# Optimization experiments

Measured on AMD Instinct MI355X. Metric: run time of the kernel, lower is better.

Reference implementation:

```python
import jax, jax.numpy as jnp
import numpy as np

TIME_SEG_LEN = 5
PRED_STEPS = 1
B, N, D = 4, 4096, 4
F1, F2 = 32, 64  # cnn filters; F2 must equal GCSConv/Dense width 64


def _conv1d_time(x, Wc1, bc1, Wc2, bc2):
    # x: [B, N, T, D] -> per-node temporal CNN collapsing T=5 -> 1 -> [B, N, F2]
    b, n, t, d = x.shape
    xr = x.reshape(b * n, t, d)
    dn = ('NWC', 'WIO', 'NWC')
    h = jax.lax.conv_general_dilated(xr, Wc1, (1,), 'VALID', dimension_numbers=dn) + bc1
    h = jax.nn.relu(h)
    h = jax.lax.conv_general_dilated(h, Wc2, (1,), 'VALID', dimension_numbers=dn) + bc2
    return h.reshape(b, n, -1)  # [B, N, F2]


def setup_inputs() -> dict:
    key = jax.random.key(0)
    ks = jax.random.split(key, 12)
    time_segs = jax.random.normal(ks[0], (B, TIME_SEG_LEN, N, D), dtype=jnp.float32)
    edges = jax.random.randint(ks[1], (N, N), 0, 2, dtype=jnp.int32)
    s = lambda *sh: 1.0 / np.sqrt(sh[-2] if len(sh) > 1 else sh[0])
    return {
        'time_segs': time_segs,
        'edges': edges,
        'Wc1': jax.random.normal(ks[2], (3, D, F1), dtype=jnp.float32) * 0.3,
        'bc1': jnp.zeros((F1,), jnp.float32),
        'Wc2': jax.random.normal(ks[3], (3, F1, F2), dtype=jnp.float32) * 0.1,
        'bc2': jnp.zeros((F2,), jnp.float32),
        'Wg1': jax.random.normal(ks[4], (F2, 64), dtype=jnp.float32) * 0.125,
        'bg': jnp.zeros((64,), jnp.float32),
        'Wd': jax.random.normal(ks[5], (F2 + 64, 64), dtype=jnp.float32) * 0.09,
        'bd': jnp.zeros((64,), jnp.float32),
        'Wo': jax.random.normal(ks[6], (64, D), dtype=jnp.float32) * 0.125,
        'bo': jnp.zeros((D,), jnp.float32),
    }


def reference(time_segs, edges, Wc1, bc1, Wc2, bc2, Wg1, bg, Wd, bd, Wo, bo):
    A = edges.astype(jnp.float32)
    n = A.shape[0]
    deg = jnp.sum(A, axis=-1, keepdims=True)              # row degree
    A_norm = A / jnp.where(deg > 0, deg, 1.0)             # D^-1 A (symmetric=False)
    A_nd = A_norm * (1.0 - jnp.eye(n, dtype=A.dtype))     # self-edge masking of X row j == zeroing diag
    col_deg = jnp.sum(A, axis=0)                          # e = np.sum(edges, axis=0)
    alive = (col_deg != 0).astype(time_segs.dtype)[None, :, None]  # zero-degree nodes -> zeros branch

    ext = jnp.transpose(time_segs, (0, 2, 1, 3))          # [B, N, T, D]
    for i in range(PRED_STEPS):
        seg = ext[:, :, i:, :]                            # [B, N, 5, D]
        cond = _conv1d_time(seg, Wc1, bc1, Wc2, bc2)      # [B, N, F2]
        # Vectorized per-node masked GCSConv: row j of tanh(A X_j W1 + X_j W2 + b)
        # with X_j = X zeroed at node j. Skip term vanishes at row j.
        agg = jnp.einsum('jk,bkf->bjf', A_nd, cond)       # [B, N, F2]
        G = jnp.tanh(agg @ Wg1 + bg) * alive              # [B, N, 64]
        h = jax.nn.relu(jnp.concatenate([cond, G], axis=-1) @ Wd + bd)
        nxt = seg[:, :, -1, :] + jnp.tanh(h @ Wo + bo)    # residual update [B, N, D]
        ext = jnp.concatenate([ext, nxt[:, :, None, :]], axis=2)
    out = jnp.transpose(ext, (0, 2, 1, 3))                # [B, T+P, N, D]
    return out[:, TIME_SEG_LEN:, :, :]                    # [B, pred_steps, N, D]
```

## Files before the change

kernel.cpp:

```cpp
#include <hip/hip_runtime.h>

typedef unsigned short ushort_t;
typedef unsigned int uint_t;
typedef unsigned long long u64_t;
typedef __attribute__((ext_vector_type(8))) __bf16 bf16x8;
typedef __attribute__((ext_vector_type(4))) float f32x4;

#define NN 4096
#define TT 5
#define F1 32
#define F2 64

__device__ __forceinline__ ushort_t f2bf(float x) {
    union { float f; uint_t u; } v; v.f = x;
    uint_t r = (v.u + 0x7FFFu + ((v.u >> 16) & 1u)) >> 16;
    return (ushort_t)r;
}
__device__ __forceinline__ float bf16f(float x) {
    union { float f; uint_t u; } v; v.f = x;
    v.u = (v.u + 0x7FFFu + ((v.u >> 16) & 1u)) & 0xFFFF0000u;
    return v.f;
}

__global__ __launch_bounds__(256) void k1_cond(
    const float* __restrict__ ts, const float* __restrict__ Wc1, const float* __restrict__ bc1,
    const float* __restrict__ Wc2, const float* __restrict__ bc2,
    float* __restrict__ condf, ushort_t* __restrict__ condT)
{
    const int b = blockIdx.y;
    const int j0 = blockIdx.x * 32;
    const int t = threadIdx.x;

    __shared__ float sWc1[384];
    __shared__ float sbc1[F1];
    __shared__ float sWc2[96 * F2];
    __shared__ float sbc2[F2];
    __shared__ float sh1[4][96];
    __shared__ ushort_t scb[64][40];

    for (int i = t; i < 384; i += 256) sWc1[i] = Wc1[i];
    for (int i = t; i < 96 * F2; i += 256) sWc2[i] = Wc2[i];
    if (t < F1) sbc1[t] = bc1[t];
    if (t < F2) sbc2[t] = bc2[t];
    __syncthreads();

    const int sub = t >> 6, lane = t & 63;
    for (int c = 0; c < 8; ++c) {
        const int n = c * 4 + sub;
        const int j = j0 + n;
        for (int idx = lane; idx < 96; idx += 64) {
            const int tt0 = idx >> 5, f1 = idx & 31;
            float a = sbc1[f1];
            #pragma unroll
            for (int dt = 0; dt < 3; ++dt) {
                const float4 x = *(const float4*)(ts + (((b * TT + tt0 + dt) * NN) + j) * 4);
                a += x.x * sWc1[(dt * 4 + 0) * F1 + f1];
                a += x.y * sWc1[(dt * 4 + 1) * F1 + f1];
                a += x.z * sWc1[(dt * 4 + 2) * F1 + f1];
                a += x.w * sWc1[(dt * 4 + 3) * F1 + f1];
            }
            sh1[sub][idx] = fmaxf(a, 0.f);
        }
        __syncthreads();
        {
            float cacc = sbc2[lane];
            #pragma unroll 8
            for (int e = 0; e < 96; ++e) cacc += sh1[sub][e] * sWc2[e * F2 + lane];
            condf[(((b << 12) + j) << 6) + lane] = cacc;
            scb[lane][n] = f2bf(cacc);
        }
        __syncthreads();
    }
    {
        const int f2 = t >> 2, seg = t & 3;
        ushort_t* dst = condT + ((size_t)(b * 64 + f2) * NN) + j0 + seg * 8;
        *(uint4*)dst = *(const uint4*)&scb[f2][seg * 8];
    }
}

__device__ __forceinline__ void stage_chunk(
    const int4 pa, int it, int kq, ushort_t* dstbuf, int soff, u64_t& regm, int& cnt)
{
    const u64_t b0 = __ballot(pa.x != 0);
    const u64_t b1 = __ballot(pa.y != 0);
    const u64_t b2 = __ballot(pa.z != 0);
    const u64_t b3 = __ballot(pa.w != 0);
    const uint_t m0 = (uint_t)(b0 | (b0 >> 32)), m1 = (uint_t)(b1 | (b1 >> 32));
    const uint_t m2 = (uint_t)(b2 | (b2 >> 32)), m3 = (uint_t)(b3 | (b3 >> 32));
    const uint_t nib = ((m0 >> kq) & 1u) | (((m1 >> kq) & 1u) << 1) |
                       (((m2 >> kq) & 1u) << 2) | (((m3 >> kq) & 1u) << 3);
    regm |= (u64_t)nib << (it * 4);
    cnt += (pa.x != 0) + (pa.y != 0) + (pa.z != 0) + (pa.w != 0);
    const uint_t h01 = (pa.x ? 0x3F80u : 0u) | (pa.y ? 0x3F800000u : 0u);
    const uint_t h23 = (pa.z ? 0x3F80u : 0u) | (pa.w ? 0x3F800000u : 0u);
    *(uint2*)(dstbuf + soff) = make_uint2(h01, h23);
}

__global__ __launch_bounds__(1024) void k3_gemm(
    const int* __restrict__ edges, const ushort_t* __restrict__ condT,
    float* __restrict__ agg0, float* __restrict__ agg1,
    int* __restrict__ degI, uint_t* __restrict__ colbits)
{
    const int t = threadIdx.x;
    const int stripe = blockIdx.x >> 1, kh = blockIdx.x & 1;
    const int j0 = stripe * 32, kb = kh * 2048;

    __shared__ __align__(16) ushort_t abuf[2][4096];
    __shared__ int degs[1024];
    __shared__ u64_t colsh[16][32];
    __shared__ u64_t colr[32];

    const int w = t >> 6, l = t & 63;
    const int r = t >> 5, kq = t & 31;
    const int rl = r & 15, rh = r >> 4;

    const int ks_s = kq >> 3, q_s = (kq >> 1) & 3;
    const int soff = (rh * 2048 + ks_s * 512 + (q_s * 16 + rl) * 8 + (kq & 1) * 4) ^ (q_s << 4);
    const int aoff = (l * 8) ^ ((l >> 4) << 4);

    const int* ep = edges + (size_t)(j0 + r) * NN + kb + kq * 4;
    const ushort_t* bp = condT + (size_t)(w * 16 + (l & 15)) * NN + kb + (l >> 4) * 8;

    u64_t regm = 0; int cnt = 0;
    int4 pa = *(const int4*)ep;
    stage_chunk(pa, 0, kq, &abuf[0][0], soff, regm, cnt);
    __syncthreads();

    f32x4 acc0 = {0.f, 0.f, 0.f, 0.f};
    f32x4 acc1 = {0.f, 0.f, 0.f, 0.f};

    for (int it = 0; it < 16; ++it) {
        if (it < 15) pa = *(const int4*)(ep + (it + 1) * 128);
        const ushort_t* ab = &abuf[it & 1][0];
        const ushort_t* bpi = bp + it * 128;
        #pragma unroll
        for (int ks = 0; ks < 4; ++ks) {
            const bf16x8 bfv = *(const bf16x8*)(bpi + ks * 32);
            const bf16x8 a0 = *(const bf16x8*)(ab + ks * 512 + aoff);
            const bf16x8 a1 = *(const bf16x8*)(ab + 2048 + ks * 512 + aoff);
            acc0 = __builtin_amdgcn_mfma_f32_16x16x32_bf16(a0, bfv, acc0, 0, 0, 0);
            acc1 = __builtin_amdgcn_mfma_f32_16x16x32_bf16(a1, bfv, acc1, 0, 0, 0);
        }
        if (it < 15) stage_chunk(pa, it + 1, kq, &abuf[(it + 1) & 1][0], soff, regm, cnt);
        __syncthreads();
    }

    {
        float* aggS = kh ? agg1 : agg0;
        const int col = w * 16 + (l & 15);
        float* dst = aggS + ((size_t)(col >> 6) * NN << 6) + (col & 63);
        #pragma unroll
        for (int i = 0; i < 4; ++i) {
            const int ja = j0 + (l >> 4) * 4 + i;
            dst[(size_t)ja << 6] = acc0[i];
            dst[(size_t)(ja + 16) << 6] = acc1[i];
        }
    }
    degs[t] = cnt;
    if (l < 32) colsh[w][kq] = regm;
    __syncthreads();
    if (t < 32) {
        u64_t v = 0;
        #pragma unroll
        for (int w2 = 0; w2 < 16; ++w2) v |= colsh[w2][t];
        colr[t] = v;
        int s = 0;
        #pragma unroll
        for (int s2 = 0; s2 < 32; ++s2) s += degs[t * 32 + s2];
        atomicAdd(&degI[j0 + t], s);
    }
    __syncthreads();
    if (t < 64) {
        uint_t word = 0;
        #pragma unroll
        for (int s = 0; s < 8; ++s) {
            const int g = (t & 3) * 8 + s;
            const uint_t nib = (uint_t)((colr[g] >> ((t >> 2) * 4)) & 15u);
            word |= nib << (s * 4);
        }
        atomicOr(&colbits[kh * 64 + t], word);
    }
}

__global__ __launch_bounds__(256) void k4_mlp(
    const float* __restrict__ ts, const int* __restrict__ edges,
    const float* __restrict__ condf,
    const float* __restrict__ agg0, const float* __restrict__ agg1,
    const int* __restrict__ degI, const uint_t* __restrict__ colbits,
    const float* __restrict__ Wg1, const float* __restrict__ bg,
    const float* __restrict__ Wd, const float* __restrict__ bd,
    const float* __restrict__ Wo, const float* __restrict__ bo,
    float* __restrict__ out)
{
    const int b = blockIdx.y;
    const int j0 = blockIdx.x * 32;
    const int t = threadIdx.x;

    __shared__ float sWg1[64 * 64];
    __shared__ float sWd[128 * 64];
    __shared__ float sWo[256];
    __shared__ float sbg[64], sbd[64], sbo[4];
    __shared__ float sAggT[64][36];
    __shared__ float sCatT[128][36];
    __shared__ float sAlive[32];

    for (int i = t; i < 64 * 64; i += 256) sWg1[i] = Wg1[i];
    for (int i = t; i < 128 * 64; i += 256) sWd[i] = Wd[i];
    if (t < 256) sWo[t] = Wo[t];
    if (t < 64) { sbg[t] = bg[t]; sbd[t] = bd[t]; }
    if (t < 4) sbo[t] = bo[t];
    if (t < 32) {
        const int j = j0 + t;
        sAlive[t] = (float)((colbits[j >> 5] >> (j & 31)) & 1u);
    }
    {
        const int n = t >> 3, fg = t & 7;
        const int j = j0 + n;
        const int dbit = edges[(size_t)j * NN + j];
        const float dv = (float)degI[j];
        const float inv = 1.f / (dv > 0.f ? dv : 1.f);
        const float dgf = dbit ? 1.f : 0.f;
        const float* ap0 = agg0 + (((size_t)(b << 12) + j) << 6) + fg * 8;
        const float* ap1 = agg1 + (((size_t)(b << 12) + j) << 6) + fg * 8;
        const float* cp = condf + (((size_t)(b << 12) + j) << 6) + fg * 8;
        #pragma unroll
        for (int i = 0; i < 2; ++i) {
            const float4 a4 = *(const float4*)(ap0 + i * 4);
            const float4 b4 = *(const float4*)(ap1 + i * 4);
            const float4 c4 = *(const float4*)(cp + i * 4);
            const int f = fg * 8 + i * 4;
            sAggT[f + 0][n] = (a4.x + b4.x - dgf * bf16f(c4.x)) * inv;  sCatT[f + 0][n] = c4.x;
            sAggT[f + 1][n] = (a4.y + b4.y - dgf * bf16f(c4.y)) * inv;  sCatT[f + 1][n] = c4.y;
            sAggT[f + 2][n] = (a4.z + b4.z - dgf * bf16f(c4.z)) * inv;  sCatT[f + 2][n] = c4.z;
            sAggT[f + 3][n] = (a4.w + b4.w - dgf * bf16f(c4.w)) * inv;  sCatT[f + 3][n] = c4.w;
        }
    }
    __syncthreads();
    {
        const int g0 = (t >> 3) * 2, n0 = (t & 7) * 4;
        float acc[2][4];
        #pragma unroll
        for (int gi = 0; gi < 2; ++gi)
            #pragma unroll
            for (int ni = 0; ni < 4; ++ni) acc[gi][ni] = sbg[g0 + gi];
        for (int e = 0; e < 64; ++e) {
            const float2 wv = *(const float2*)&sWg1[(e << 6) + g0];
            const float4 av = *(const float4*)&sAggT[e][n0];
            const float aa[4] = {av.x, av.y, av.z, av.w};
            #pragma unroll
            for (int ni = 0; ni < 4; ++ni) { acc[0][ni] += wv.x * aa[ni]; acc[1][ni] += wv.y * aa[ni]; }
        }
        #pragma unroll
        for (int gi = 0; gi < 2; ++gi)
            #pragma unroll
            for (int ni = 0; ni < 4; ++ni)
                sCatT[64 + g0 + gi][n0 + ni] = tanhf(acc[gi][ni]) * sAlive[n0 + ni];
    }
    __syncthreads();
    {
        const int h0 = (t >> 3) * 2, n0 = (t & 7) * 4;
        float acc[2][4];
        #pragma unroll
        for (int hi = 0; hi < 2; ++hi)
            #pragma unroll
            for (int ni = 0; ni < 4; ++ni) acc[hi][ni] = sbd[h0 + hi];
        for (int e = 0; e < 128; ++e) {
            const float2 wv = *(const float2*)&sWd[(e << 6) + h0];
            const float4 av = *(const float4*)&sCatT[e][n0];
            const float aa[4] = {av.x, av.y, av.z, av.w};
            #pragma unroll
            for (int ni = 0; ni < 4; ++ni) { acc[0][ni] += wv.x * aa[ni]; acc[1][ni] += wv.y * aa[ni]; }
        }
        __syncthreads();
        #pragma unroll
        for (int hi = 0; hi < 2; ++hi)
            #pragma unroll
            for (int ni = 0; ni < 4; ++ni)
                sAggT[h0 + hi][n0 + ni] = fmaxf(acc[hi][ni], 0.f);
    }
    __syncthreads();
    if (t < 128) {
        const int d = t >> 5, n = t & 31;
        const int j = j0 + n;
        float s = sbo[d];
        #pragma unroll 8
        for (int f = 0; f < 64; ++f) s += sAggT[f][n] * sWo[f * 4 + d];
        const float segl = ts[(((b * TT + 4) * NN) + j) * 4 + d];
        out[((((size_t)b << 12) + j) << 2) + d] = segl + tanhf(s);
    }
}

extern "C" void kernel_launch(void* const* d_in, const int* in_sizes, int n_in,
                              void* d_out, int out_size, void* d_ws, size_t ws_size,
                              hipStream_t stream)
{
    (void)in_sizes; (void)n_in; (void)out_size; (void)ws_size;
    const float* ts    = (const float*)d_in[0];
    const int*   edges = (const int*)d_in[1];
    const float* Wc1   = (const float*)d_in[2];
    const float* bc1   = (const float*)d_in[3];
    const float* Wc2   = (const float*)d_in[4];
    const float* bc2   = (const float*)d_in[5];
    const float* Wg1   = (const float*)d_in[6];
    const float* bg    = (const float*)d_in[7];
    const float* Wd    = (const float*)d_in[8];
    const float* bd    = (const float*)d_in[9];
    const float* Wo    = (const float*)d_in[10];
    const float* bo    = (const float*)d_in[11];
    float* out = (float*)d_out;

    char* ws = (char*)d_ws;
    ushort_t* condT   = (ushort_t*)(ws);
    float*    condf   = (float*)(ws + (size_t)(2 << 20));
    float*    agg0    = (float*)(ws + (size_t)(6 << 20));
    float*    agg1    = (float*)(ws + (size_t)(10 << 20));
    int*      degI    = (int*)(ws + (size_t)(14 << 20));
    uint_t*   colbits = (uint_t*)(ws + (size_t)(14 << 20) + 16384);

    hipMemsetAsync(degI, 0, 16384 + 512, stream);

    k1_cond<<<dim3(128, 4), 256, 0, stream>>>(ts, Wc1, bc1, Wc2, bc2, condf, condT);
    k3_gemm<<<256, 1024, 0, stream>>>(edges, condT, agg0, agg1, degI, colbits);
    k4_mlp<<<dim3(128, 4), 256, 0, stream>>>(ts, edges, condf, agg0, agg1, degI, colbits,
                                             Wg1, bg, Wd, bd, Wo, bo, out);
}
```

Baseline: 200.1 us.

## Move conv and MLP dense layers in k1/k4 onto bf16 MFMA

Rewrites the second temporal conv in k1 and the GCS/Dense matmuls in k4 as bf16 MFMA 16x16x32 tiles, with transposed bf16 weights staged in shared memory. Each block now handles 64 nodes, so the grid is halved. tanhf is replaced with an exp/rcp approximation. The aim is to cut scalar FMA and LDS time in the small kernels, at the cost of bf16 rounding of activations and weights, which adds precision error.

After: 165.6 us. 1.21x faster.

```diff
diff --git a/kernel.cpp b/kernel.cpp
--- a/kernel.cpp
+++ b/kernel.cpp
@@ -1,4 +1,5 @@
 #include <hip/hip_runtime.h>
+#include <math.h>
 
 typedef unsigned short ushort_t;
 typedef unsigned int uint_t;
@@ -21,60 +22,99 @@
     v.u = (v.u + 0x7FFFu + ((v.u >> 16) & 1u)) & 0xFFFF0000u;
     return v.f;
 }
-
+__device__ __forceinline__ uint_t pk2(float a, float b) {
+    return (uint_t)f2bf(a) | ((uint_t)f2bf(b) << 16);
+}
+__device__ __forceinline__ float tanh_fast(float x) {
+    const float xc = fminf(fmaxf(x, -10.f), 10.f);
+    const float e = __expf(2.f * xc);
+    return (e - 1.f) * __builtin_amdgcn_rcpf(e + 1.f);
+}
+
+#define H1S 104
+#define CBS 80
 __global__ __launch_bounds__(256) void k1_cond(
     const float* __restrict__ ts, const float* __restrict__ Wc1, const float* __restrict__ bc1,
     const float* __restrict__ Wc2, const float* __restrict__ bc2,
     float* __restrict__ condf, ushort_t* __restrict__ condT)
 {
     const int b = blockIdx.y;
-    const int j0 = blockIdx.x * 32;
+    const int j0 = blockIdx.x * 64;
     const int t = threadIdx.x;
 
     __shared__ float sWc1[384];
     __shared__ float sbc1[F1];
-    __shared__ float sWc2[96 * F2];
     __shared__ float sbc2[F2];
-    __shared__ float sh1[4][96];
-    __shared__ ushort_t scb[64][40];
+    __shared__ ushort_t sWc2T[64 * H1S];
+    __shared__ ushort_t h1B[64 * H1S];
+    __shared__ ushort_t scb[64 * CBS];
 
     for (int i = t; i < 384; i += 256) sWc1[i] = Wc1[i];
-    for (int i = t; i < 96 * F2; i += 256) sWc2[i] = Wc2[i];
     if (t < F1) sbc1[t] = bc1[t];
     if (t < F2) sbc2[t] = bc2[t];
-    __syncthreads();
-
-    const int sub = t >> 6, lane = t & 63;
-    for (int c = 0; c < 8; ++c) {
-        const int n = c * 4 + sub;
+    for (int i = t; i < 96 * 64; i += 256) {
+        const int e = i >> 6, f = i & 63;
+        sWc2T[f * H1S + e] = f2bf(Wc2[i]);
+    }
+    __syncthreads();
+
+    {
+        const int n = t & 63, f10 = (t >> 6) * 8;
         const int j = j0 + n;
-        for (int idx = lane; idx < 96; idx += 64) {
-            const int tt0 = idx >> 5, f1 = idx & 31;
-            float a = sbc1[f1];
-            #pragma unroll
-            for (int dt = 0; dt < 3; ++dt) {
-                const float4 x = *(const float4*)(ts + (((b * TT + tt0 + dt) * NN) + j) * 4);
-                a += x.x * sWc1[(dt * 4 + 0) * F1 + f1];
-                a += x.y * sWc1[(dt * 4 + 1) * F1 + f1];
-                a += x.z * sWc1[(dt * 4 + 2) * F1 + f1];
-                a += x.w * sWc1[(dt * 4 + 3) * F1 + f1];
-            }
-            sh1[sub][idx] = fmaxf(a, 0.f);
-        }
-        __syncthreads();
-        {
-            float cacc = sbc2[lane];
-            #pragma unroll 8
-            for (int e = 0; e < 96; ++e) cacc += sh1[sub][e] * sWc2[e * F2 + lane];
-            condf[(((b << 12) + j) << 6) + lane] = cacc;
-            scb[lane][n] = f2bf(cacc);
-        }
-        __syncthreads();
-    }
+        float4 x[5];
+        #pragma unroll
+        for (int tt = 0; tt < 5; ++tt)
+            x[tt] = *(const float4*)(ts + ((((size_t)b * TT + tt) << 12) + j) * 4);
+        #pragma unroll
+        for (int tt0 = 0; tt0 < 3; ++tt0) {
+            #pragma unroll
+            for (int ff = 0; ff < 8; ++ff) {
+                const int f1 = f10 + ff;
+                float a = sbc1[f1];
+                #pragma unroll
+                for (int dt = 0; dt < 3; ++dt) {
+                    const float4 xx = x[tt0 + dt];
+                    a += xx.x * sWc1[(dt * 4 + 0) * F1 + f1];
+                    a += xx.y * sWc1[(dt * 4 + 1) * F1 + f1];
+                    a += xx.z * sWc1[(dt * 4 + 2) * F1 + f1];
+                    a += xx.w * sWc1[(dt * 4 + 3) * F1 + f1];
+                }
+                h1B[n * H1S + tt0 * 32 + f1] = f2bf(fmaxf(a, 0.f));
+            }
+        }
+    }
+    __syncthreads();
+
+    {
+        const int w = t >> 6, l = t & 63;
+        const int m0 = w * 16, kseg = (l >> 4) * 8;
+        f32x4 acc[4] = {};
+        #pragma unroll
+        for (int ks = 0; ks < 3; ++ks) {
+            const bf16x8 av = *(const bf16x8*)&h1B[(m0 + (l & 15)) * H1S + ks * 32 + kseg];
+            #pragma unroll
+            for (int ct = 0; ct < 4; ++ct) {
+                const bf16x8 bv = *(const bf16x8*)&sWc2T[(ct * 16 + (l & 15)) * H1S + ks * 32 + kseg];
+                acc[ct] = __builtin_amdgcn_mfma_f32_16x16x32_bf16(av, bv, acc[ct], 0, 0, 0);
+            }
+        }
+        #pragma unroll
+        for (int ct = 0; ct < 4; ++ct)
+            #pragma unroll
+            for (int i = 0; i < 4; ++i) {
+                const int row = m0 + (l >> 4) * 4 + i;
+                const int col = ct * 16 + (l & 15);
+                const float c = acc[ct][i] + sbc2[col];
+                condf[((((size_t)b << 12) + j0 + row) << 6) + col] = c;
+                scb[col * CBS + row] = f2bf(c);
+            }
+    }
+    __syncthreads();
     {
         const int f2 = t >> 2, seg = t & 3;
-        ushort_t* dst = condT + ((size_t)(b * 64 + f2) * NN) + j0 + seg * 8;
-        *(uint4*)dst = *(const uint4*)&scb[f2][seg * 8];
+        ushort_t* dst = condT + (((size_t)b * 64 + f2) << 12) + j0 + seg * 16;
+        *(uint4*)dst = *(const uint4*)&scb[f2 * CBS + seg * 16];
+        *(uint4*)(dst + 8) = *(const uint4*)&scb[f2 * CBS + seg * 16 + 8];
     }
 }
 
@@ -182,6 +222,9 @@
     }
 }
 
+#define WGS 88
+#define WDS 136
+#define HS  69
 __global__ __launch_bounds__(256) void k4_mlp(
     const float* __restrict__ ts, const int* __restrict__ edges,
     const float* __restrict__ condf,
@@ -193,100 +236,109 @@
     float* __restrict__ out)
 {
     const int b = blockIdx.y;
-    const int j0 = blockIdx.x * 32;
+    const int j0 = blockIdx.x * 64;
     const int t = threadIdx.x;
 
-    __shared__ float sWg1[64 * 64];
-    __shared__ float sWd[128 * 64];
+    __shared__ ushort_t sWg1T[64 * WGS];
+    __shared__ ushort_t sWdT[64 * WDS];
+    __shared__ ushort_t aggB[64 * WGS];
+    __shared__ ushort_t catB[64 * WDS];
+    __shared__ float sH[64 * HS];
     __shared__ float sWo[256];
-    __shared__ float sbg[64], sbd[64], sbo[4];
-    __shared__ float sAggT[64][36];
-    __shared__ float sCatT[128][36];
-    __shared__ float sAlive[32];
-
-    for (int i = t; i < 64 * 64; i += 256) sWg1[i] = Wg1[i];
-    for (int i = t; i < 128 * 64; i += 256) sWd[i] = Wd[i];
+    __shared__ float sbg[64], sbd[64], sbo[4], sAlive[64];
+
+    for (int i = t; i < 4096; i += 256) {
+        const int in = i >> 6, o = i & 63;
+        sWg1T[o * WGS + in] = f2bf(Wg1[i]);
+    }
+    for (int i = t; i < 8192; i += 256) {
+        const int in = i >> 6, o = i & 63;
+        sWdT[o * WDS + in] = f2bf(Wd[i]);
+    }
     if (t < 256) sWo[t] = Wo[t];
     if (t < 64) { sbg[t] = bg[t]; sbd[t] = bd[t]; }
     if (t < 4) sbo[t] = bo[t];
-    if (t < 32) {
+    if (t < 64) {
         const int j = j0 + t;
         sAlive[t] = (float)((colbits[j >> 5] >> (j & 31)) & 1u);
     }
     {
-        const int n = t >> 3, fg = t & 7;
-        const int j = j0 + n;
-        const int dbit = edges[(size_t)j * NN + j];
+        const int r = t >> 2, fs = t & 3;
+        const int j = j0 + r;
         const float dv = (float)degI[j];
         const float inv = 1.f / (dv > 0.f ? dv : 1.f);
-        const float dgf = dbit ? 1.f : 0.f;
-        const float* ap0 = agg0 + (((size_t)(b << 12) + j) << 6) + fg * 8;
-        const float* ap1 = agg1 + (((size_t)(b << 12) + j) << 6) + fg * 8;
-        const float* cp = condf + (((size_t)(b << 12) + j) << 6) + fg * 8;
-        #pragma unroll
-        for (int i = 0; i < 2; ++i) {
-            const float4 a4 = *(const float4*)(ap0 + i * 4);
-            const float4 b4 = *(const float4*)(ap1 + i * 4);
-            const float4 c4 = *(const float4*)(cp + i * 4);
-            const int f = fg * 8 + i * 4;
-            sAggT[f + 0][n] = (a4.x + b4.x - dgf * bf16f(c4.x)) * inv;  sCatT[f + 0][n] = c4.x;
-            sAggT[f + 1][n] = (a4.y + b4.y - dgf * bf16f(c4.y)) * inv;  sCatT[f + 1][n] = c4.y;
-            sAggT[f + 2][n] = (a4.z + b4.z - dgf * bf16f(c4.z)) * inv;  sCatT[f + 2][n] = c4.z;
-            sAggT[f + 3][n] = (a4.w + b4.w - dgf * bf16f(c4.w)) * inv;  sCatT[f + 3][n] = c4.w;
-        }
-    }
-    __syncthreads();
-    {
-        const int g0 = (t >> 3) * 2, n0 = (t & 7) * 4;
-        float acc[2][4];
-        #pragma unroll
-        for (int gi = 0; gi < 2; ++gi)
-            #pragma unroll
-            for (int ni = 0; ni < 4; ++ni) acc[gi][ni] = sbg[g0 + gi];
-        for (int e = 0; e < 64; ++e) {
-            const float2 wv = *(const float2*)&sWg1[(e << 6) + g0];
-            const float4 av = *(const float4*)&sAggT[e][n0];
-            const float aa[4] = {av.x, av.y, av.z, av.w};
-            #pragma unroll
-            for (int ni = 0; ni < 4; ++ni) { acc[0][ni] += wv.x * aa[ni]; acc[1][ni] += wv.y * aa[ni]; }
-        }
-        #pragma unroll
-        for (int gi = 0; gi < 2; ++gi)
-            #pragma unroll
-            for (int ni = 0; ni < 4; ++ni)
-                sCatT[64 + g0 + gi][n0 + ni] = tanhf(acc[gi][ni]) * sAlive[n0 + ni];
-    }
-    __syncthreads();
-    {
-        const int h0 = (t >> 3) * 2, n0 = (t & 7) * 4;
-        float acc[2][4];
-        #pragma unroll
-        for (int hi = 0; hi < 2; ++hi)
-            #pragma unroll
-            for (int ni = 0; ni < 4; ++ni) acc[hi][ni] = sbd[h0 + hi];
-        for (int e = 0; e < 128; ++e) {
-            const float2 wv = *(const float2*)&sWd[(e << 6) + h0];
-            const float4 av = *(const float4*)&sCatT[e][n0];
-            const float aa[4] = {av.x, av.y, av.z, av.w};
-            #pragma unroll
-            for (int ni = 0; ni < 4; ++ni) { acc[0][ni] += wv.x * aa[ni]; acc[1][ni] += wv.y * aa[ni]; }
-        }
-        __syncthreads();
-        #pragma unroll
-        for (int hi = 0; hi < 2; ++hi)
-            #pragma unroll
-            for (int ni = 0; ni < 4; ++ni)
-                sAggT[h0 + hi][n0 + ni] = fmaxf(acc[hi][ni], 0.f);
-    }
-    __syncthreads();
-    if (t < 128) {
-        const int d = t >> 5, n = t & 31;
-        const int j = j0 + n;
+        const float dgf = edges[(size_t)j * NN + j] ? 1.f : 0.f;
+        const size_t base = (((size_t)b << 12) + j) << 6;
+        #pragma unroll
+        for (int q = 0; q < 4; ++q) {
+            const int f = fs * 16 + q * 4;
+            const float4 a0 = *(const float4*)(agg0 + base + f);
+            const float4 a1 = *(const float4*)(agg1 + base + f);
+            const float4 c4 = *(const float4*)(condf + base + f);
+            const float n0 = (a0.x + a1.x - dgf * bf16f(c4.x)) * inv;
+            const float n1 = (a0.y + a1.y - dgf * bf16f(c4.y)) * inv;
+            const float n2 = (a0.z + a1.z - dgf * bf16f(c4.z)) * inv;
+            const float n3 = (a0.w + a1.w - dgf * bf16f(c4.w)) * inv;
+            *(uint2*)&aggB[r * WGS + f] = make_uint2(pk2(n0, n1), pk2(n2, n3));
+            *(uint2*)&catB[r * WDS + f] = make_uint2(pk2(c4.x, c4.y), pk2(c4.z, c4.w));
+        }
+    }
+    __syncthreads();
+
+    const int w = t >> 6, l = t & 63;
+    const int m0 = w * 16, kseg = (l >> 4) * 8;
+
+    {
+        f32x4 acc[4] = {};
+        #pragma unroll
+        for (int ks = 0; ks < 2; ++ks) {
+            const bf16x8 av = *(const bf16x8*)&aggB[(m0 + (l & 15)) * WGS + ks * 32 + kseg];
+            #pragma unroll
+            for (int ct = 0; ct < 4; ++ct) {
+                const bf16x8 bv = *(const bf16x8*)&sWg1T[(ct * 16 + (l & 15)) * WGS + ks * 32 + kseg];
+                acc[ct] = __builtin_amdgcn_mfma_f32_16x16x32_bf16(av, bv, acc[ct], 0, 0, 0);
+            }
+        }
+        #pragma unroll
+        for (int ct = 0; ct < 4; ++ct)
+            #pragma unroll
+            for (int i = 0; i < 4; ++i) {
+                const int row = m0 + (l >> 4) * 4 + i;
+                const int col = ct * 16 + (l & 15);
+                const float g = tanh_fast(acc[ct][i] + sbg[col]) * sAlive[row];
+                catB[row * WDS + 64 + col] = f2bf(g);
+            }
+    }
+    __syncthreads();
+    {
+        f32x4 acc[4] = {};
+        #pragma unroll
+        for (int ks = 0; ks < 4; ++ks) {
+            const bf16x8 av = *(const bf16x8*)&catB[(m0 + (l & 15)) * WDS + ks * 32 + kseg];
+            #pragma unroll
+            for (int ct = 0; ct < 4; ++ct) {
+                const bf16x8 bv = *(const bf16x8*)&sWdT[(ct * 16 + (l & 15)) * WDS + ks * 32 + kseg];
+                acc[ct] = __builtin_amdgcn_mfma_f32_16x16x32_bf16(av, bv, acc[ct], 0, 0, 0);
+            }
+        }
+        #pragma unroll
+        for (int ct = 0; ct < 4; ++ct)
+            #pragma unroll
+            for (int i = 0; i < 4; ++i) {
+                const int row = m0 + (l >> 4) * 4 + i;
+                const int col = ct * 16 + (l & 15);
+                sH[row * HS + col] = fmaxf(acc[ct][i] + sbd[col], 0.f);
+            }
+    }
+    __syncthreads();
+    {
+        const int r = t >> 2, d = t & 3;
+        const int j = j0 + r;
         float s = sbo[d];
         #pragma unroll 8
-        for (int f = 0; f < 64; ++f) s += sAggT[f][n] * sWo[f * 4 + d];
-        const float segl = ts[(((b * TT + 4) * NN) + j) * 4 + d];
-        out[((((size_t)b << 12) + j) << 2) + d] = segl + tanhf(s);
+        for (int f = 0; f < 64; ++f) s += sH[r * HS + f] * sWo[f * 4 + d];
+        const float segl = ts[((((size_t)b * TT + 4) << 12) + j) * 4 + d];
+        out[((((size_t)b << 12) + j) << 2) + d] = segl + tanh_fast(s);
     }
 }
 
@@ -319,8 +371,8 @@
 
     hipMemsetAsync(degI, 0, 16384 + 512, stream);
 
-    k1_cond<<<dim3(128, 4), 256, 0, stream>>>(ts, Wc1, bc1, Wc2, bc2, condf, condT);
+    k1_cond<<<dim3(64, 4), 256, 0, stream>>>(ts, Wc1, bc1, Wc2, bc2, condf, condT);
     k3_gemm<<<256, 1024, 0, stream>>>(edges, condT, agg0, agg1, degI, colbits);
-    k4_mlp<<<dim3(128, 4), 256, 0, stream>>>(ts, edges, condf, agg0, agg1, degI, colbits,
-                                             Wg1, bg, Wd, bd, Wo, bo, out);
-}
+    k4_mlp<<<dim3(64, 4), 256, 0, stream>>>(ts, edges, condf, agg0, agg1, degI, colbits,
+                                            Wg1, bg, Wd, bd, Wo, bo, out);
+}
```
